# Kernel tuning notes

Hardware: AMD Instinct MI355X
Metric: run time of the kernel (lower is better)

Reference implementation:

```python
import jax, jax.numpy as jnp
import numpy as np

N_HEAD = 4

def setup_inputs() -> dict:
    key = jax.random.key(0)
    ks = jax.random.split(key, 5)
    B, T, C = 2, 4096, 64
    return {
        "x": jax.random.normal(ks[0], (B, T, C), dtype=jnp.float32),
        "w_attn": jax.random.normal(ks[1], (3 * C, C), dtype=jnp.float32) * 0.02,
        "b_attn": jax.random.normal(ks[2], (3 * C,), dtype=jnp.float32) * 0.02,
        "w_proj": jax.random.normal(ks[3], (C, C), dtype=jnp.float32) * 0.02,
        "b_proj": jax.random.normal(ks[4], (C,), dtype=jnp.float32) * 0.02,
    }

def reference(x, w_attn, b_attn, w_proj, b_proj):
    B, T, C = x.shape
    H = N_HEAD
    Dh = C // H
    # fused QKV projection (torch Linear: x @ W.T + b)
    qkv = x @ w_attn.T + b_attn                      # [B,T,3C]
    q, k, v = jnp.split(qkv, 3, axis=-1)             # each [B,T,C]
    q = q.reshape(B, T, H, Dh).transpose(0, 2, 1, 3)  # [B,H,T,Dh]
    k = k.reshape(B, T, H, Dh).transpose(0, 2, 1, 3)
    v = v.reshape(B, T, H, Dh).transpose(0, 2, 1, 3)
    scale = 1.0 / np.sqrt(Dh).astype(np.float32)
    scores = jnp.einsum("bhqd,bhkd->bhqk", q, k) * scale  # [B,H,T,T]
    attn = jax.nn.softmax(scores, axis=-1)
    y = jnp.einsum("bhqk,bhkd->bhqd", attn, v)       # [B,H,T,Dh]
    y = y.transpose(0, 2, 1, 3).reshape(B, T, C)     # [B,T,C]
    return y @ w_proj.T + b_proj
```

## Files before the change

kernel.cpp:

```cpp
#include <hip/hip_runtime.h>
#include <math.h>

#define BB 2
#define TT 4096
#define CC 64
#define HH 4
#define DH 16
#define NROW (BB*TT)
#define SCALE 0.36067376022224085f

typedef __fp16 h4 __attribute__((ext_vector_type(4)));
typedef __fp16 h2 __attribute__((ext_vector_type(2)));
typedef __fp16 h8 __attribute__((ext_vector_type(8)));
typedef float  f4 __attribute__((ext_vector_type(4)));
typedef float  f16v __attribute__((ext_vector_type(16)));

union U4H8 { uint4 u; h8 h; };
union UWH8 { unsigned u[4]; h8 h; };

__global__ __launch_bounds__(256) void qkv_kernel(const float* __restrict__ x,
        const float* __restrict__ w, const float* __restrict__ bias,
        __fp16* __restrict__ Q, __fp16* __restrict__ K, __fp16* __restrict__ VT) {
    __shared__ __fp16 smv[64][16];
    const int t = threadIdx.x;
    const int wave = t >> 6, lane = t & 63;
    const int lq = lane & 15, g = lane >> 4;
    const int r0 = blockIdx.x*16;
    const int b = r0 >> 12, tt0 = r0 & (TT-1);

    h4 xb[4];
    const float* xrow = x + (size_t)(r0 + lq)*CC;
    #pragma unroll
    for (int s = 0; s < 4; s++) {
        float4 xv = *(const float4*)(xrow + s*16 + g*4);
        h2 lo = __builtin_amdgcn_cvt_pkrtz(xv.x, xv.y);
        h2 hi = __builtin_amdgcn_cvt_pkrtz(xv.z, xv.w);
        xb[s] = (h4){lo.x, lo.y, hi.x, hi.y};
    }

    #pragma unroll
    for (int j = 0; j < 3; j++) {
        const int nt = wave*3 + j;
        const int o0 = nt*16;
        const float sc = (nt < 4) ? SCALE : 1.0f;
        float4 bv = *(const float4*)(bias + o0 + g*4);
        f4 acc = {bv.x*sc, bv.y*sc, bv.z*sc, bv.w*sc};
        #pragma unroll
        for (int s = 0; s < 4; s++) {
            float4 wv = *(const float4*)(w + (size_t)(o0 + lq)*CC + s*16 + g*4);
            h2 lo = __builtin_amdgcn_cvt_pkrtz(wv.x*sc, wv.y*sc);
            h2 hi = __builtin_amdgcn_cvt_pkrtz(wv.z*sc, wv.w*sc);
            h4 af = (h4){lo.x, lo.y, hi.x, hi.y};
            acc = __builtin_amdgcn_mfma_f32_16x16x16f16(af, xb[s], acc, 0, 0, 0);
        }
        h2 plo = __builtin_amdgcn_cvt_pkrtz(acc.x, acc.y);
        h2 phi = __builtin_amdgcn_cvt_pkrtz(acc.z, acc.w);
        h4 pk = (h4){plo.x, plo.y, phi.x, phi.y};
        if (nt < 8) {
            const int part = nt >> 2, h = nt & 3;
            __fp16* dst = (part == 0) ? Q : K;
            *(h4*)(dst + ((size_t)(b*HH + h)*TT + tt0 + lq)*DH + g*4) = pk;
        } else {
            const int h = nt - 8;
            smv[h*16 + g*4 + 0][lq] = pk.x;
            smv[h*16 + g*4 + 1][lq] = pk.y;
            smv[h*16 + g*4 + 2][lq] = pk.z;
            smv[h*16 + g*4 + 3][lq] = pk.w;
        }
    }
    __syncthreads();
    if (t < 64) {
        const int h = t >> 4, d = t & 15;
        uint4 v0 = *(const uint4*)&smv[t][0];
        uint4 v1 = *(const uint4*)&smv[t][8];
        uint4 pa = {v0.x, v0.y, v1.x, v1.y};
        uint4 pb = {v0.z, v0.w, v1.z, v1.w};
        __fp16* dst = VT + (size_t)(b*HH + h)*TT*32
                        + (size_t)(tt0 >> 6)*2048
                        + (size_t)((tt0 & 63) >> 4)*512
                        + (size_t)d*16;
        *(uint4*)dst = pa;
        *(uint4*)(dst + 8) = pb;
        const unsigned cb = (d == 0 || d == 4) ? 0x3C003C00u : 0u;
        const uint4 cv = {cb, cb, cb, cb};
        __fp16* dst2 = dst + 16*16;
        *(uint4*)dst2 = cv;
        *(uint4*)(dst2 + 8) = cv;
    }
}

__global__ __launch_bounds__(256) void attn_kernel(const __fp16* __restrict__ Q,
        const __fp16* __restrict__ K, const __fp16* __restrict__ VT,
        __fp16* __restrict__ yh) {
    __shared__ float Osm[4][2][64][9];
    const int t = threadIdx.x;
    const int wave = t >> 6, lane = t & 63;
    const int l31 = lane & 31, hi = lane >> 5;
    const int head = blockIdx.x & 7;
    const int qt   = blockIdx.x >> 3;
    const int q0 = qt*64;
    const __fp16* Qh = Q  + (size_t)head*TT*DH;
    const __fp16* Kh = K  + (size_t)head*TT*DH;
    const __fp16* Vh = VT + (size_t)head*TT*32;

    U4H8 qf0, qf1;
    qf0.u = *(const uint4*)(Qh + (size_t)(q0 + l31)*DH + hi*8);
    qf1.u = *(const uint4*)(Qh + (size_t)(q0 + 32 + l31)*DH + hi*8);

    const f16v Zf = {0.f,0.f,0.f,0.f,0.f,0.f,0.f,0.f,0.f,0.f,0.f,0.f,0.f,0.f,0.f,0.f};
    f16v O0 = Zf, O1 = Zf;

    const __fp16* kbase = Kh + (size_t)(wave*1024 + l31)*DH + hi*8;
    const __fp16* vbase = Vh + (size_t)(wave*16)*2048 + l31*16 + hi*8;

    const int start = (blockIdx.x*5 + wave*3) & 15;

    uint4 ka[2], va[4], kb[2], vb[4];

#define LOADC(c, KF, VF)                                                   \
    {  const size_t cc_ = (size_t)(c);                                     \
       _Pragma("unroll") for (int kt_ = 0; kt_ < 2; kt_++)                 \
           KF[kt_] = *(const uint4*)(kbase + cc_*1024 + kt_*512);          \
       _Pragma("unroll") for (int s_ = 0; s_ < 4; s_++)                    \
           VF[s_] = *(const uint4*)(vbase + cc_*2048 + s_*512);            \
    }

    LOADC(start, ka, va)

#define PROC_TILE(S, O, VF)                                                        \
    {   float p_[16]; unsigned W_[8];                                              \
        _Pragma("unroll") for (int r_ = 0; r_ < 16; r_++)                          \
            p_[r_] = __builtin_amdgcn_exp2f(S[r_]);                                \
        _Pragma("unroll") for (int m_ = 0; m_ < 8; m_++)                           \
            W_[m_] = __builtin_bit_cast(unsigned,                                  \
                __builtin_amdgcn_cvt_pkrtz(p_[2*m_], p_[2*m_+1]));                 \
        _Pragma("unroll") for (int s2 = 0; s2 < 2; s2++) {                         \
            UWH8 bw_;                                                              \
            bw_.u[0] = W_[4*s2+0];  bw_.u[1] = W_[4*s2+1];                         \
            bw_.u[2] = W_[4*s2+2];  bw_.u[3] = W_[4*s2+3];                         \
            U4H8 vv_; vv_.u = VF[kt*2+s2];                                         \
            O = __builtin_amdgcn_mfma_f32_32x32x16_f16(vv_.h, bw_.h, O, 0,0,0);    \
        }                                                                          \
    }

#define ATTN_CHUNK(KF, VF)                                                         \
    _Pragma("unroll")                                                              \
    for (int kt = 0; kt < 2; kt++) {                                               \
        U4H8 ak_; ak_.u = KF[kt];                                                  \
        f16v S0 = __builtin_amdgcn_mfma_f32_32x32x16_f16(ak_.h, qf0.h, Zf, 0,0,0); \
        f16v S1 = __builtin_amdgcn_mfma_f32_32x32x16_f16(ak_.h, qf1.h, Zf, 0,0,0); \
        PROC_TILE(S0, O0, VF)                                                      \
        PROC_TILE(S1, O1, VF)                                                      \
    }

    for (int it = 0; it < 16; it += 2) {
        LOADC((start + it + 1) & 15, kb, vb)
        ATTN_CHUNK(ka, va)
        LOADC((start + it + 2) & 15, ka, va)
        ATTN_CHUNK(kb, vb)
    }
#undef ATTN_CHUNK
#undef PROC_TILE
#undef LOADC

    #pragma unroll
    for (int r = 0; r < 9; r++) {
        Osm[wave][0][lane][r] = O0[r];
        Osm[wave][1][lane][r] = O1[r];
    }
    __syncthreads();
    if (wave < 2) {
        const int qt2 = wave;
        float a[9];
        #pragma unroll
        for (int r = 0; r < 9; r++)
            a[r] = Osm[0][qt2][lane][r] + Osm[1][qt2][lane][r]
                 + Osm[2][qt2][lane][r] + Osm[3][qt2][lane][r];
        const float rinv = 1.f / a[8];
        h2 plo = __builtin_amdgcn_cvt_pkrtz(a[0]*rinv, a[1]*rinv);
        h2 phi = __builtin_amdgcn_cvt_pkrtz(a[2]*rinv, a[3]*rinv);
        h4 pk1 = (h4){plo.x, plo.y, phi.x, phi.y};
        plo = __builtin_amdgcn_cvt_pkrtz(a[4]*rinv, a[5]*rinv);
        phi = __builtin_amdgcn_cvt_pkrtz(a[6]*rinv, a[7]*rinv);
        h4 pk2 = (h4){plo.x, plo.y, phi.x, phi.y};
        const int b = head >> 2, hh = head & 3;
        const size_t q = (size_t)q0 + qt2*32 + l31;
        __fp16* dst = yh + ((size_t)b*TT + q)*CC + hh*DH + hi*4;
        *(h4*)dst = pk1;
        *(h4*)(dst + 8) = pk2;
    }
}

__global__ __launch_bounds__(256) void proj_kernel(const __fp16* __restrict__ yh,
        const float* __restrict__ w, const float* __restrict__ bias,
        float* __restrict__ out) {
    const int t = threadIdx.x;
    const int wave = t >> 6, lane = t & 63;
    const int lq = lane & 15, g = lane >> 4;
    const int r0 = blockIdx.x*16;
    const int o0 = wave*16;

    h4 yb[4];
    const __fp16* yrow = yh + (size_t)(r0 + lq)*CC;
    #pragma unroll
    for (int s = 0; s < 4; s++) yb[s] = *(const h4*)(yrow + s*16 + g*4);

    float4 bv = *(const float4*)(bias + o0 + g*4);
    f4 acc = {bv.x, bv.y, bv.z, bv.w};
    #pragma unroll
    for (int s = 0; s < 4; s++) {
        float4 wv = *(const float4*)(w + (size_t)(o0 + lq)*CC + s*16 + g*4);
        h2 lo = __builtin_amdgcn_cvt_pkrtz(wv.x, wv.y);
        h2 hi = __builtin_amdgcn_cvt_pkrtz(wv.z, wv.w);
        h4 af = (h4){lo.x, lo.y, hi.x, hi.y};
        acc = __builtin_amdgcn_mfma_f32_16x16x16f16(af, yb[s], acc, 0, 0, 0);
    }
    *(float4*)(out + (size_t)(r0 + lq)*CC + o0 + g*4) = (float4){acc.x, acc.y, acc.z, acc.w};
}

extern "C" void kernel_launch(void* const* d_in, const int* in_sizes, int n_in,
                              void* d_out, int out_size, void* d_ws, size_t ws_size,
                              hipStream_t stream) {
    const float* x      = (const float*)d_in[0];
    const float* w_attn = (const float*)d_in[1];
    const float* b_attn = (const float*)d_in[2];
    const float* w_proj = (const float*)d_in[3];
    const float* b_proj = (const float*)d_in[4];
    float* out = (float*)d_out;

    const size_t headszQK = (size_t)BB*HH*TT*DH;
    const size_t vtsz     = (size_t)BB*HH*TT*32;
    __fp16* Q   = (__fp16*)d_ws;
    __fp16* K   = Q + headszQK;
    __fp16* VT  = K + headszQK;
    __fp16* yh  = VT + vtsz;

    qkv_kernel<<<NROW/16, 256, 0, stream>>>(x, w_attn, b_attn, Q, K, VT);
    attn_kernel<<<BB*HH*(TT/64), 256, 0, stream>>>(Q, K, VT, yh);
    proj_kernel<<<NROW/16, 256, 0, stream>>>(yh, w_proj, b_proj, out);
}
```

Before: 88.71 us.

## Fuse QKV, attention and projection into one kernel with software grid barriers

Merges the three launches into one 512-block kernel that separates the phases with a global atomic grid barrier, and shares the LDS buffers through a union. The aim is to remove launch gaps and tail effects between the QKV, attention and projection stages. It relies on all 512 blocks being resident at once, since this is an ordinary launch rather than a cooperative one, so it can deadlock if occupancy drops. The barrier's atomics and spinning also add synchronisation cost.

After: 336.8 us. 280% more time.

```diff
diff --git a/kernel.cpp b/kernel.cpp
--- a/kernel.cpp
+++ b/kernel.cpp
@@ -7,6 +7,7 @@
 #define HH 4
 #define DH 16
 #define NROW (BB*TT)
+#define NBLK (NROW/16)
 #define SCALE 0.36067376022224085f
 
 typedef __fp16 h4 __attribute__((ext_vector_type(4)));
@@ -18,104 +19,138 @@
 union U4H8 { uint4 u; h8 h; };
 union UWH8 { unsigned u[4]; h8 h; };
 
-__global__ __launch_bounds__(256) void qkv_kernel(const float* __restrict__ x,
-        const float* __restrict__ w, const float* __restrict__ bias,
-        __fp16* __restrict__ Q, __fp16* __restrict__ K, __fp16* __restrict__ VT) {
-    __shared__ __fp16 smv[64][16];
+__device__ unsigned bar_count = 0;
+__device__ unsigned bar_gen   = 0;
+
+__device__ __forceinline__ void grid_barrier() {
+    __syncthreads();
+    __threadfence();
+    if (threadIdx.x == 0) {
+        unsigned gen = __hip_atomic_load(&bar_gen, __ATOMIC_ACQUIRE,
+                                         __HIP_MEMORY_SCOPE_AGENT);
+        unsigned arrived = __hip_atomic_fetch_add(&bar_count, 1u, __ATOMIC_ACQ_REL,
+                                                  __HIP_MEMORY_SCOPE_AGENT) + 1u;
+        if (arrived == (unsigned)NBLK) {
+            __hip_atomic_store(&bar_count, 0u, __ATOMIC_RELAXED,
+                               __HIP_MEMORY_SCOPE_AGENT);
+            __hip_atomic_store(&bar_gen, gen + 1u, __ATOMIC_RELEASE,
+                               __HIP_MEMORY_SCOPE_AGENT);
+        } else {
+            while (__hip_atomic_load(&bar_gen, __ATOMIC_ACQUIRE,
+                                     __HIP_MEMORY_SCOPE_AGENT) == gen)
+                __builtin_amdgcn_s_sleep(2);
+        }
+    }
+    __threadfence();
+    __syncthreads();
+}
+
+__global__ __launch_bounds__(256, 2) void fused_kernel(
+        const float* __restrict__ x,
+        const float* __restrict__ w_attn, const float* __restrict__ b_attn,
+        const float* __restrict__ w_proj, const float* __restrict__ b_proj,
+        float* __restrict__ out,
+        __fp16* __restrict__ Q, __fp16* __restrict__ K,
+        __fp16* __restrict__ VT, __fp16* __restrict__ yh)
+{
+    __shared__ union {
+        __fp16 smv[64][16];
+        float  Osm[4][2][64][9];
+    } sh;
+
     const int t = threadIdx.x;
     const int wave = t >> 6, lane = t & 63;
     const int lq = lane & 15, g = lane >> 4;
-    const int r0 = blockIdx.x*16;
-    const int b = r0 >> 12, tt0 = r0 & (TT-1);
-
-    h4 xb[4];
-    const float* xrow = x + (size_t)(r0 + lq)*CC;
-    #pragma unroll
-    for (int s = 0; s < 4; s++) {
-        float4 xv = *(const float4*)(xrow + s*16 + g*4);
-        h2 lo = __builtin_amdgcn_cvt_pkrtz(xv.x, xv.y);
-        h2 hi = __builtin_amdgcn_cvt_pkrtz(xv.z, xv.w);
-        xb[s] = (h4){lo.x, lo.y, hi.x, hi.y};
-    }
-
-    #pragma unroll
-    for (int j = 0; j < 3; j++) {
-        const int nt = wave*3 + j;
-        const int o0 = nt*16;
-        const float sc = (nt < 4) ? SCALE : 1.0f;
-        float4 bv = *(const float4*)(bias + o0 + g*4);
-        f4 acc = {bv.x*sc, bv.y*sc, bv.z*sc, bv.w*sc};
+
+    {
+        const int r0 = blockIdx.x*16;
+        const int b = r0 >> 12, tt0 = r0 & (TT-1);
+
+        h4 xb[4];
+        const float* xrow = x + (size_t)(r0 + lq)*CC;
         #pragma unroll
         for (int s = 0; s < 4; s++) {
-            float4 wv = *(const float4*)(w + (size_t)(o0 + lq)*CC + s*16 + g*4);
-            h2 lo = __builtin_amdgcn_cvt_pkrtz(wv.x*sc, wv.y*sc);
-            h2 hi = __builtin_amdgcn_cvt_pkrtz(wv.z*sc, wv.w*sc);
-            h4 af = (h4){lo.x, lo.y, hi.x, hi.y};
-            acc = __builtin_amdgcn_mfma_f32_16x16x16f16(af, xb[s], acc, 0, 0, 0);
-        }
-        h2 plo = __builtin_amdgcn_cvt_pkrtz(acc.x, acc.y);
-        h2 phi = __builtin_amdgcn_cvt_pkrtz(acc.z, acc.w);
-        h4 pk = (h4){plo.x, plo.y, phi.x, phi.y};
-        if (nt < 8) {
-            const int part = nt >> 2, h = nt & 3;
-            __fp16* dst = (part == 0) ? Q : K;
-            *(h4*)(dst + ((size_t)(b*HH + h)*TT + tt0 + lq)*DH + g*4) = pk;
-        } else {
-            const int h = nt - 8;
-            smv[h*16 + g*4 + 0][lq] = pk.x;
-            smv[h*16 + g*4 + 1][lq] = pk.y;
-            smv[h*16 + g*4 + 2][lq] = pk.z;
-            smv[h*16 + g*4 + 3][lq] = pk.w;
-        }
-    }
-    __syncthreads();
-    if (t < 64) {
-        const int h = t >> 4, d = t & 15;
-        uint4 v0 = *(const uint4*)&smv[t][0];
-        uint4 v1 = *(const uint4*)&smv[t][8];
-        uint4 pa = {v0.x, v0.y, v1.x, v1.y};
-        uint4 pb = {v0.z, v0.w, v1.z, v1.w};
-        __fp16* dst = VT + (size_t)(b*HH + h)*TT*32
-                        + (size_t)(tt0 >> 6)*2048
-                        + (size_t)((tt0 & 63) >> 4)*512
-                        + (size_t)d*16;
-        *(uint4*)dst = pa;
-        *(uint4*)(dst + 8) = pb;
-        const unsigned cb = (d == 0 || d == 4) ? 0x3C003C00u : 0u;
-        const uint4 cv = {cb, cb, cb, cb};
-        __fp16* dst2 = dst + 16*16;
-        *(uint4*)dst2 = cv;
-        *(uint4*)(dst2 + 8) = cv;
-    }
-}
-
-__global__ __launch_bounds__(256) void attn_kernel(const __fp16* __restrict__ Q,
-        const __fp16* __restrict__ K, const __fp16* __restrict__ VT,
-        __fp16* __restrict__ yh) {
-    __shared__ float Osm[4][2][64][9];
-    const int t = threadIdx.x;
-    const int wave = t >> 6, lane = t & 63;
-    const int l31 = lane & 31, hi = lane >> 5;
-    const int head = blockIdx.x & 7;
-    const int qt   = blockIdx.x >> 3;
-    const int q0 = qt*64;
-    const __fp16* Qh = Q  + (size_t)head*TT*DH;
-    const __fp16* Kh = K  + (size_t)head*TT*DH;
-    const __fp16* Vh = VT + (size_t)head*TT*32;
-
-    U4H8 qf0, qf1;
-    qf0.u = *(const uint4*)(Qh + (size_t)(q0 + l31)*DH + hi*8);
-    qf1.u = *(const uint4*)(Qh + (size_t)(q0 + 32 + l31)*DH + hi*8);
-
-    const f16v Zf = {0.f,0.f,0.f,0.f,0.f,0.f,0.f,0.f,0.f,0.f,0.f,0.f,0.f,0.f,0.f,0.f};
-    f16v O0 = Zf, O1 = Zf;
-
-    const __fp16* kbase = Kh + (size_t)(wave*1024 + l31)*DH + hi*8;
-    const __fp16* vbase = Vh + (size_t)(wave*16)*2048 + l31*16 + hi*8;
-
-    const int start = (blockIdx.x*5 + wave*3) & 15;
-
-    uint4 ka[2], va[4], kb[2], vb[4];
+            float4 xv = *(const float4*)(xrow + s*16 + g*4);
+            h2 lo = __builtin_amdgcn_cvt_pkrtz(xv.x, xv.y);
+            h2 hi = __builtin_amdgcn_cvt_pkrtz(xv.z, xv.w);
+            xb[s] = (h4){lo.x, lo.y, hi.x, hi.y};
+        }
+
+        #pragma unroll
+        for (int j = 0; j < 3; j++) {
+            const int nt = wave*3 + j;
+            const int o0 = nt*16;
+            const float sc = (nt < 4) ? SCALE : 1.0f;
+            float4 bv = *(const float4*)(b_attn + o0 + g*4);
+            f4 acc = {bv.x*sc, bv.y*sc, bv.z*sc, bv.w*sc};
+            #pragma unroll
+            for (int s = 0; s < 4; s++) {
+                float4 wv = *(const float4*)(w_attn + (size_t)(o0 + lq)*CC + s*16 + g*4);
+                h2 lo = __builtin_amdgcn_cvt_pkrtz(wv.x*sc, wv.y*sc);
+                h2 hi = __builtin_amdgcn_cvt_pkrtz(wv.z*sc, wv.w*sc);
+                h4 af = (h4){lo.x, lo.y, hi.x, hi.y};
+                acc = __builtin_amdgcn_mfma_f32_16x16x16f16(af, xb[s], acc, 0, 0, 0);
+            }
+            h2 plo = __builtin_amdgcn_cvt_pkrtz(acc.x, acc.y);
+            h2 phi = __builtin_amdgcn_cvt_pkrtz(acc.z, acc.w);
+            h4 pk = (h4){plo.x, plo.y, phi.x, phi.y};
+            if (nt < 8) {
+                const int part = nt >> 2, h = nt & 3;
+                __fp16* dst = (part == 0) ? Q : K;
+                *(h4*)(dst + ((size_t)(b*HH + h)*TT + tt0 + lq)*DH + g*4) = pk;
+            } else {
+                const int h = nt - 8;
+                sh.smv[h*16 + g*4 + 0][lq] = pk.x;
+                sh.smv[h*16 + g*4 + 1][lq] = pk.y;
+                sh.smv[h*16 + g*4 + 2][lq] = pk.z;
+                sh.smv[h*16 + g*4 + 3][lq] = pk.w;
+            }
+        }
+        __syncthreads();
+        if (t < 64) {
+            const int h = t >> 4, d = t & 15;
+            uint4 v0 = *(const uint4*)&sh.smv[t][0];
+            uint4 v1 = *(const uint4*)&sh.smv[t][8];
+            uint4 pa = {v0.x, v0.y, v1.x, v1.y};
+            uint4 pb = {v0.z, v0.w, v1.z, v1.w};
+            __fp16* dst = VT + (size_t)(b*HH + h)*TT*32
+                            + (size_t)(tt0 >> 6)*2048
+                            + (size_t)((tt0 & 63) >> 4)*512
+                            + (size_t)d*16;
+            *(uint4*)dst = pa;
+            *(uint4*)(dst + 8) = pb;
+            const unsigned cb = (d == 0 || d == 4) ? 0x3C003C00u : 0u;
+            const uint4 cv = {cb, cb, cb, cb};
+            __fp16* dst2 = dst + 16*16;
+            *(uint4*)dst2 = cv;
+            *(uint4*)(dst2 + 8) = cv;
+        }
+    }
+
+    grid_barrier();
+
+    {
+        const int l31 = lane & 31, hi = lane >> 5;
+        const int head = blockIdx.x & 7;
+        const int qt   = blockIdx.x >> 3;
+        const int q0 = qt*64;
+        const __fp16* Qh = Q  + (size_t)head*TT*DH;
+        const __fp16* Kh = K  + (size_t)head*TT*DH;
+        const __fp16* Vh = VT + (size_t)head*TT*32;
+
+        U4H8 qf0, qf1;
+        qf0.u = *(const uint4*)(Qh + (size_t)(q0 + l31)*DH + hi*8);
+        qf1.u = *(const uint4*)(Qh + (size_t)(q0 + 32 + l31)*DH + hi*8);
+
+        const f16v Zf = {0.f,0.f,0.f,0.f,0.f,0.f,0.f,0.f,0.f,0.f,0.f,0.f,0.f,0.f,0.f,0.f};
+        f16v O0 = Zf, O1 = Zf;
+
+        const __fp16* kbase = Kh + (size_t)(wave*1024 + l31)*DH + hi*8;
+        const __fp16* vbase = Vh + (size_t)(wave*16)*2048 + l31*16 + hi*8;
+
+        const int start = (blockIdx.x*5 + wave*3) & 15;
+
+        uint4 ka[2], va[4], kb[2], vb[4];
 
 #define LOADC(c, KF, VF)                                                   \
     {  const size_t cc_ = (size_t)(c);                                     \
@@ -125,7 +160,7 @@
            VF[s_] = *(const uint4*)(vbase + cc_*2048 + s_*512);            \
     }
 
-    LOADC(start, ka, va)
+        LOADC(start, ka, va)
 
 #define PROC_TILE(S, O, VF)                                                        \
     {   float p_[16]; unsigned W_[8];                                              \
@@ -153,69 +188,68 @@
         PROC_TILE(S1, O1, VF)                                                      \
     }
 
-    for (int it = 0; it < 16; it += 2) {
-        LOADC((start + it + 1) & 15, kb, vb)
-        ATTN_CHUNK(ka, va)
-        LOADC((start + it + 2) & 15, ka, va)
-        ATTN_CHUNK(kb, vb)
-    }
+        for (int it = 0; it < 16; it += 2) {
+            LOADC((start + it + 1) & 15, kb, vb)
+            ATTN_CHUNK(ka, va)
+            LOADC((start + it + 2) & 15, ka, va)
+            ATTN_CHUNK(kb, vb)
+        }
 #undef ATTN_CHUNK
 #undef PROC_TILE
 #undef LOADC
 
-    #pragma unroll
-    for (int r = 0; r < 9; r++) {
-        Osm[wave][0][lane][r] = O0[r];
-        Osm[wave][1][lane][r] = O1[r];
-    }
-    __syncthreads();
-    if (wave < 2) {
-        const int qt2 = wave;
-        float a[9];
-        #pragma unroll
-        for (int r = 0; r < 9; r++)
-            a[r] = Osm[0][qt2][lane][r] + Osm[1][qt2][lane][r]
-                 + Osm[2][qt2][lane][r] + Osm[3][qt2][lane][r];
-        const float rinv = 1.f / a[8];
-        h2 plo = __builtin_amdgcn_cvt_pkrtz(a[0]*rinv, a[1]*rinv);
-        h2 phi = __builtin_amdgcn_cvt_pkrtz(a[2]*rinv, a[3]*rinv);
-        h4 pk1 = (h4){plo.x, plo.y, phi.x, phi.y};
-        plo = __builtin_amdgcn_cvt_pkrtz(a[4]*rinv, a[5]*rinv);
-        phi = __builtin_amdgcn_cvt_pkrtz(a[6]*rinv, a[7]*rinv);
-        h4 pk2 = (h4){plo.x, plo.y, phi.x, phi.y};
-        const int b = head >> 2, hh = head & 3;
-        const size_t q = (size_t)q0 + qt2*32 + l31;
-        __fp16* dst = yh + ((size_t)b*TT + q)*CC + hh*DH + hi*4;
-        *(h4*)dst = pk1;
-        *(h4*)(dst + 8) = pk2;
-    }
-}
-
-__global__ __launch_bounds__(256) void proj_kernel(const __fp16* __restrict__ yh,
-        const float* __restrict__ w, const float* __restrict__ bias,
-        float* __restrict__ out) {
-    const int t = threadIdx.x;
-    const int wave = t >> 6, lane = t & 63;
-    const int lq = lane & 15, g = lane >> 4;
-    const int r0 = blockIdx.x*16;
-    const int o0 = wave*16;
-
-    h4 yb[4];
-    const __fp16* yrow = yh + (size_t)(r0 + lq)*CC;
-    #pragma unroll
-    for (int s = 0; s < 4; s++) yb[s] = *(const h4*)(yrow + s*16 + g*4);
-
-    float4 bv = *(const float4*)(bias + o0 + g*4);
-    f4 acc = {bv.x, bv.y, bv.z, bv.w};
-    #pragma unroll
-    for (int s = 0; s < 4; s++) {
-        float4 wv = *(const float4*)(w + (size_t)(o0 + lq)*CC + s*16 + g*4);
-        h2 lo = __builtin_amdgcn_cvt_pkrtz(wv.x, wv.y);
-        h2 hi = __builtin_amdgcn_cvt_pkrtz(wv.z, wv.w);
-        h4 af = (h4){lo.x, lo.y, hi.x, hi.y};
-        acc = __builtin_amdgcn_mfma_f32_16x16x16f16(af, yb[s], acc, 0, 0, 0);
-    }
-    *(float4*)(out + (size_t)(r0 + lq)*CC + o0 + g*4) = (float4){acc.x, acc.y, acc.z, acc.w};
+        __syncthreads();
+        #pragma unroll
+        for (int r = 0; r < 9; r++) {
+            sh.Osm[wave][0][lane][r] = O0[r];
+            sh.Osm[wave][1][lane][r] = O1[r];
+        }
+        __syncthreads();
+        if (wave < 2) {
+            const int qt2 = wave;
+            float a[9];
+            #pragma unroll
+            for (int r = 0; r < 9; r++)
+                a[r] = sh.Osm[0][qt2][lane][r] + sh.Osm[1][qt2][lane][r]
+                     + sh.Osm[2][qt2][lane][r] + sh.Osm[3][qt2][lane][r];
+            const float rinv = 1.f / a[8];
+            h2 plo = __builtin_amdgcn_cvt_pkrtz(a[0]*rinv, a[1]*rinv);
+            h2 phi = __builtin_amdgcn_cvt_pkrtz(a[2]*rinv, a[3]*rinv);
+            h4 pk1 = (h4){plo.x, plo.y, phi.x, phi.y};
+            plo = __builtin_amdgcn_cvt_pkrtz(a[4]*rinv, a[5]*rinv);
+            phi = __builtin_amdgcn_cvt_pkrtz(a[6]*rinv, a[7]*rinv);
+            h4 pk2 = (h4){plo.x, plo.y, phi.x, phi.y};
+            const int b = head >> 2, hh = head & 3;
+            const size_t q = (size_t)q0 + qt2*32 + l31;
+            __fp16* dst = yh + ((size_t)b*TT + q)*CC + hh*DH + hi*4;
+            *(h4*)dst = pk1;
+            *(h4*)(dst + 8) = pk2;
+        }
+    }
+
+    grid_barrier();
+
+    {
+        const int r0 = blockIdx.x*16;
+        const int o0 = wave*16;
+
+        h4 yb[4];
+        const __fp16* yrow = yh + (size_t)(r0 + lq)*CC;
+        #pragma unroll
+        for (int s = 0; s < 4; s++) yb[s] = *(const h4*)(yrow + s*16 + g*4);
+
+        float4 bv = *(const float4*)(b_proj + o0 + g*4);
+        f4 acc = {bv.x, bv.y, bv.z, bv.w};
+        #pragma unroll
+        for (int s = 0; s < 4; s++) {
+            float4 wv = *(const float4*)(w_proj + (size_t)(o0 + lq)*CC + s*16 + g*4);
+            h2 lo = __builtin_amdgcn_cvt_pkrtz(wv.x, wv.y);
+            h2 hi = __builtin_amdgcn_cvt_pkrtz(wv.z, wv.w);
+            h4 af = (h4){lo.x, lo.y, hi.x, hi.y};
+            acc = __builtin_amdgcn_mfma_f32_16x16x16f16(af, yb[s], acc, 0, 0, 0);
+        }
+        *(float4*)(out + (size_t)(r0 + lq)*CC + o0 + g*4) = (float4){acc.x, acc.y, acc.z, acc.w};
+    }
 }
 
 extern "C" void kernel_launch(void* const* d_in, const int* in_sizes, int n_in,
@@ -235,7 +269,6 @@
     __fp16* VT  = K + headszQK;
     __fp16* yh  = VT + vtsz;
 
-    qkv_kernel<<<NROW/16, 256, 0, stream>>>(x, w_attn, b_attn, Q, K, VT);
-    attn_kernel<<<BB*HH*(TT/64), 256, 0, stream>>>(Q, K, VT, yh);
-    proj_kernel<<<NROW/16, 256, 0, stream>>>(yh, w_proj, b_proj, out);
+    fused_kernel<<<NBLK, 256, 0, stream>>>(x, w_attn, b_attn, w_proj, b_proj,
+                                           out, Q, K, VT, yh);
 }
```
